# Kernel tuning notes

Measured on AMD Instinct MI355X. Metric: run time of the kernel, lower is better.

The kernel has to match this reference:

```python
import jax, jax.numpy as jnp
import numpy as np
from jax import lax

G = 64      # ngroup
CPN = 4     # channels per group in hidden layers
H, W = 32, 64
K = 5       # conv kernel
BIN = 8     # bin_num
BIAS = 3.5  # (bin_num-1)/2
NMIX = 3    # GMM components (batch replicas)
SCALE = 65536.0


def _group_mask(cout, cin, strict):
    # wavefront causality: tap (dg, di, dj) allowed iff dg+di+dj < 0 (strict) or <= 0
    g = jnp.arange(G)
    dg = g[None, :] - g[:, None]                      # (Gout, Gin)
    off = jnp.arange(K) - K // 2
    dd = off[:, None] + off[None, :]                  # (K, K)
    tot = dg[:, :, None, None] + dd[None, None, :, :]
    m = (tot < 0) if strict else (tot <= 0)
    m = jnp.repeat(jnp.repeat(m, cout, axis=0), cin, axis=1)
    return m.astype(jnp.float32)                      # (G*cout, G*cin, K, K)


def _cconv(x, w, b, m, relu):
    y = lax.conv_general_dilated(x, w * m, (1, 1), 'SAME',
                                 dimension_numbers=('NCHW', 'OIHW', 'NCHW'))
    y = y + b[None, :, None, None]
    return jax.nn.relu(y) if relu else y


def setup_inputs() -> dict:
    key = jax.random.key(0)
    ks = jax.random.split(key, 8)
    data = jax.random.randint(ks[0], (1, G, H, W), 0, BIN).astype(jnp.float32)
    mask = jax.random.randint(ks[1], (1, G, H, W), 0, 2).astype(jnp.float32)
    s = 0.05
    w_in = jax.random.normal(ks[2], (G * CPN, G, K, K), jnp.float32) * s
    b_in = jnp.zeros((G * CPN,), jnp.float32)
    w_hid = jax.random.normal(ks[3], (10, G * CPN, G * CPN, K, K), jnp.float32) * s
    b_hid = jnp.zeros((10, G * CPN), jnp.float32)
    w_out = jax.random.normal(ks[4], (G * NMIX, G * CPN, K, K), jnp.float32) * s
    b_out = jnp.zeros((G * NMIX,), jnp.float32)
    return dict(data=data, mask=mask, w_in=w_in, b_in=b_in,
                w_hid=w_hid, b_hid=b_hid, w_out=w_out, b_out=b_out)


def reference(data, mask, w_in, b_in, w_hid, b_hid, w_out, b_out):
    m_in = _group_mask(CPN, 1, True)      # first layer: strict (excludes current group)
    m_hid = _group_mask(CPN, CPN, False)
    m_out = _group_mask(NMIX, CPN, False)
    tdata = (data - BIAS) * mask
    x = jnp.concatenate([tdata, tdata, tdata], axis=0)   # (3, G, H, W)
    x = _cconv(x, w_in, b_in, m_in, True)
    for i in range(5):                                   # 5 residual blocks
        h = _cconv(x, w_hid[2 * i], b_hid[2 * i], m_hid, True)
        h = _cconv(h, w_hid[2 * i + 1], b_hid[2 * i + 1], m_hid, True)
        x = x + h
    y = _cconv(x, w_out, b_out, m_out, False)            # (3, G*3, H, W)
    y = y.reshape(NMIX, G, NMIX, H, W)                   # batch replica m -> mixture m
    logits = y[:, :, 0]
    mu = y[:, :, 1]
    sig = jax.nn.softplus(y[:, :, 2]) + 1e-6
    wts = jax.nn.softmax(logits, axis=0)                 # (3, G, H, W)
    edges = jnp.arange(BIN, dtype=jnp.float32) + 0.5 - BIAS
    z = (edges[:, None, None, None, None] - mu[None]) / (sig[None] * jnp.float32(np.sqrt(2.0)))
    cdf = 0.5 * (1.0 + lax.erf(z))                       # (BIN, 3, G, H, W)
    table = jnp.einsum('kmghw,mghw->ghwk', cdf, wts) * SCALE
    return table                                         # (G, H, W, BIN) quantizable CDF
```

## Files before the change

kernel.cpp:

```cpp
#include <hip/hip_runtime.h>
#include <math.h>

typedef _Float16 f16;
typedef _Float16 f16x8 __attribute__((ext_vector_type(8)));
typedef float f32x4 __attribute__((ext_vector_type(4)));

#define HH 32
#define WW 64
#define NPX 2048
#define SLOTS 68
#define CHS 78336
#define LOSCALE 2048.0f
#define INV_LOSCALE 4.8828125e-4f

typedef const __attribute__((address_space(1))) void gvoid;
typedef __attribute__((address_space(3))) void lvoid;
__device__ __forceinline__ void gload_lds16(const void* g, void* l) {
    __builtin_amdgcn_global_load_lds((gvoid*)g, (lvoid*)l, 16, 0, 0);
}

__global__ void zero_kernel(f16* p, int n8) {
    int i = blockIdx.x * 256 + threadIdx.x;
    if (i < n8) *(int4*)(p + i * 8) = make_int4(0, 0, 0, 0);
}

__global__ void prep_kernel(const float* __restrict__ data,
                            const float* __restrict__ mask,
                            f16* __restrict__ X0, int plane) {
    int idx = blockIdx.x * 256 + threadIdx.x;
    if (idx >= NPX * 64) return;
    int px = idx >> 6, ci = idx & 63;
    int hh = px >> 6, w = px & 63;
    float v = (data[ci * NPX + px] - 3.5f) * mask[ci * NPX + px];
    int dst = (ci >> 5) * CHS + ((hh + 2) * SLOTS + (w + 2)) * 32 + (ci & 31);
    X0[dst] = (f16)v;
    X0[plane + dst] = (f16)0.f;
}

__global__ void repack_kernel(const float* __restrict__ W, f16* __restrict__ WP,
                              int cin_log2, int coutp_log2,
                              int cpg_in_log2, int limb, int is_out) {
    int idx = blockIdx.x * 256 + threadIdx.x;
    int Cin = 1 << cin_log2;
    int plane = 25 << (cin_log2 + coutp_log2);
    int ci = idx & (Cin - 1);
    int rest = idx >> cin_log2;
    int co_p = rest & ((1 << coutp_log2) - 1);
    int tap = rest >> coutp_log2;
    if (tap >= 25) return;
    int ky = tap / 5, kx = tap - 5 * ky;
    int co_orig, g_out;
    if (is_out) { g_out = co_p >> 1; co_orig = 3 * g_out + 1 + (co_p & 1); }
    else        { g_out = co_p >> 2; co_orig = co_p; }
    int g_in = ci >> cpg_in_log2;
    float v = 0.f;
    if (ky + kx <= limb + g_out - g_in)
        v = W[(co_orig * Cin + ci) * 25 + tap];
    f16 vh = (f16)v;
    int dst = (((tap << (coutp_log2 - 4)) + (co_p >> 4)) << (cin_log2 - 5 + 9))
            + ((ci >> 5) << 9) + ((co_p & 15) << 5) + (ci & 31);
    WP[dst] = vh;
    WP[plane + dst] = (f16)((v - (float)vh) * LOSCALE);
}

__global__ __launch_bounds__(320, 3) void conv_kernel(
    const f16* __restrict__ IN, int Cin, int inPlane,
    const f16* __restrict__ WP, int wPlane,
    const float* __restrict__ bias,
    const f16* __restrict__ RES, int resPlane,
    f16* __restrict__ OA, int oaPlane,
    float* __restrict__ OT,
    int nmt, int Coutp, int cpg_out, int cpg_in, int limb, int mode)
{
    __shared__ __align__(16) char SMEM[46080];
    f16* BL = (f16*)SMEM;
    float* RED = (float*)SMEM;

    const int t = threadIdx.x;
    const int kw = t >> 6;
    const int lane = t & 63, l15 = lane & 15, q = lane >> 4;

    int b = blockIdx.x;
    int half = nmt << 4;
    int slot = b >= half ? 1 : 0;
    int idx = b - (slot ? half : 0);
    int mt8 = idx >> 5;
    const int h = idx & 31;
    const int mt = slot ? (nmt - 1 - mt8) : mt8;
    const int co0 = mt * 16;
    const int g_max = (co0 + 15) / cpg_out;

    int cnt[5];
#pragma unroll
    for (int kx = 0; kx < 5; kx++) {
        int c = (g_max + limb - (kw + kx) + 1) * cpg_in;
        c = c < Cin ? c : Cin;
        cnt[kx] = c > 0 ? c : 0;
    }
    int ci_top = (g_max + limb + 1) * cpg_in;
    ci_top = ci_top < Cin ? ci_top : Cin;

    const f16* src[9];
#pragma unroll
    for (int r = 0; r < 9; r++) {
        int u = r * 320 + t;
        if (u >= 2720) u = 0;
        int pl = u >= 1360 ? 1 : 0;
        int rem = u - pl * 1360;
        src[r] = IN + (size_t)pl * inPlane + h * 2176 + rem * 8;
    }

    f32x4 acc_h[4], acc_m[4];
#pragma unroll
    for (int j = 0; j < 4; j++) {
        acc_h[j] = (f32x4){0.f, 0.f, 0.f, 0.f};
        acc_m[j] = (f32x4){0.f, 0.f, 0.f, 0.f};
    }

    const size_t kxs = (size_t)Coutp * Cin;
    const f16* wb0 = WP + (size_t)(kw * 5 * (Coutp >> 4) + mt) * ((size_t)Cin << 4)
                   + l15 * 32 + q * 8;

    int coff = 0;
    for (int ci0 = 0; ci0 < ci_top; ci0 += 32, coff += CHS) {
        __syncthreads();
#pragma unroll
        for (int r = 0; r < 9; r++) {
            int ub = r * 320 + kw * 64;
            if (ub < 2720)
                gload_lds16(src[r] + coff, BL + ub * 8);
        }
        __syncthreads();

        const f16* wb = wb0 + (ci0 >> 5) * 512;
        f16x8 cah, cal, nah, nal;
        if (ci0 < cnt[0]) {
            cah = *(const f16x8*)(wb);
            cal = *(const f16x8*)(wb + wPlane);
        }
#pragma unroll
        for (int kx = 0; kx < 5; kx++) {
            if (ci0 >= cnt[kx]) break;
            if (kx < 4 && ci0 < cnt[kx + 1]) {
                nah = *(const f16x8*)(wb + (kx + 1) * kxs);
                nal = *(const f16x8*)(wb + (kx + 1) * kxs + wPlane);
            }
            f16x8 bh[4], bl[4];
#pragma unroll
            for (int j = 0; j < 4; j++) {
                int slt = j * 16 + l15 + kx;
                bh[j] = *(const f16x8*)&BL[(0 * 5 + kw) * (SLOTS * 32) + slt * 32 + q * 8];
                bl[j] = *(const f16x8*)&BL[(1 * 5 + kw) * (SLOTS * 32) + slt * 32 + q * 8];
            }
#pragma unroll
            for (int j = 0; j < 4; j++) {
                acc_h[j] = __builtin_amdgcn_mfma_f32_16x16x32_f16(cah, bh[j], acc_h[j], 0, 0, 0);
                acc_m[j] = __builtin_amdgcn_mfma_f32_16x16x32_f16(cah, bl[j], acc_m[j], 0, 0, 0);
                acc_m[j] = __builtin_amdgcn_mfma_f32_16x16x32_f16(cal, bh[j], acc_m[j], 0, 0, 0);
            }
            cah = nah; cal = nal;
        }
    }

    __syncthreads();
#pragma unroll
    for (int j = 0; j < 4; j++) {
        f32x4 v;
#pragma unroll
        for (int r = 0; r < 4; r++)
            v[r] = acc_h[j][r] + acc_m[j][r] * INV_LOSCALE;
        *(f32x4*)&RED[(kw * 64 + j * 16 + l15) * 20 + q * 4] = v;
    }
    __syncthreads();

    if (mode == 0) {
        for (int c = t; c < 1024; c += 320) {
            int px = c >> 4, col = c & 15;
            float v = bias[co0 + col];
#pragma unroll
            for (int k5 = 0; k5 < 5; k5++) v += RED[(k5 * 64 + px) * 20 + col];
            v = fmaxf(v, 0.f);
            int cc = co0 + col;
            int o = (cc >> 5) * CHS + ((h + 2) * SLOTS + px + 2) * 32 + (cc & 31);
            if (RES) v += (float)RES[o] + (float)RES[resPlane + o] * INV_LOSCALE;
            f16 vh = (f16)v;
            OA[o] = vh;
            OA[oaPlane + o] = (f16)((v - (float)vh) * LOSCALE);
        }
    } else {
        for (int c = t; c < 1024; c += 320) {
            int px = c >> 4, col = c & 15;
            float v = bias[3 * ((co0 + col) >> 1) + 1 + (col & 1)];
#pragma unroll
            for (int k5 = 0; k5 < 5; k5++) v += RED[(k5 * 64 + px) * 20 + col];
            RED[px * 20 + col] = v;
        }
        __syncthreads();
        for (int c = t; c < 512; c += 320) {
            int px = c >> 3, gl = c & 7;
            float mu = RED[px * 20 + 2 * gl];
            float s  = RED[px * 20 + 2 * gl + 1];
            float sp = fmaxf(s, 0.f) + log1pf(expf(-fabsf(s)));
            float sig = sp + 1e-6f;
            float inv = 1.f / (sig * 1.41421356237f);
            int g = (co0 >> 1) + gl;
            float* o = OT + ((size_t)g * NPX + h * WW + px) * 8;
#pragma unroll
            for (int k = 0; k < 8; k++) {
                float z = ((float)k - 3.0f - mu) * inv;
                o[k] = 32768.f * (1.f + erff(z));
            }
        }
    }
}

extern "C" void kernel_launch(void* const* d_in, const int* in_sizes, int n_in,
                              void* d_out, int out_size, void* d_ws, size_t ws_size,
                              hipStream_t stream) {
    const float* data  = (const float*)d_in[0];
    const float* mask  = (const float*)d_in[1];
    const float* w_in  = (const float*)d_in[2];
    const float* b_in  = (const float*)d_in[3];
    const float* w_hid = (const float*)d_in[4];
    const float* b_hid = (const float*)d_in[5];
    const float* w_out = (const float*)d_in[6];
    const float* b_out = (const float*)d_in[7];
    float* out = (float*)d_out;

    f16* WP = (f16*)d_ws;
    f16* P  = WP + 3276800;
    f16* Q  = P + 1253376;
    f16* X0 = Q + 1253376;

    zero_kernel<<<1377, 256, 0, stream>>>(P, 352512);
    prep_kernel<<<512, 256, 0, stream>>>(data, mask, X0, 156672);

    repack_kernel<<<1600, 256, 0, stream>>>(w_in, WP, 6, 8, 0, 3, 0);
    conv_kernel<<<512, 320, 0, stream>>>(X0, 64, 156672, WP, 409600,
        b_in, nullptr, 0, P, 626688, nullptr, 16, 256, 4, 1, 3, 0);

    for (int i = 0; i < 5; i++) {
        repack_kernel<<<6400, 256, 0, stream>>>(w_hid + (size_t)(2 * i) * 1638400,
                                                WP, 8, 8, 2, 4, 0);
        conv_kernel<<<512, 320, 0, stream>>>(P, 256, 626688, WP, 1638400,
            b_hid + 2 * i * 256, nullptr, 0, Q, 626688, nullptr, 16, 256, 4, 4, 4, 0);
        repack_kernel<<<6400, 256, 0, stream>>>(w_hid + (size_t)(2 * i + 1) * 1638400,
                                                WP, 8, 8, 2, 4, 0);
        conv_kernel<<<512, 320, 0, stream>>>(Q, 256, 626688, WP, 1638400,
            b_hid + (2 * i + 1) * 256, P, 626688, P, 626688, nullptr, 16, 256, 4, 4, 4, 0);
    }

    repack_kernel<<<3200, 256, 0, stream>>>(w_out, WP, 8, 7, 2, 4, 1);
    conv_kernel<<<256, 320, 0, stream>>>(P, 256, 626688, WP, 819200,
        b_out, nullptr, 0, nullptr, 0, out, 8, 128, 2, 4, 4, 1);
}
```

Baseline: 459.7 us.

## Pair complementary output tiles per block and double-buffer input loads

```diff
diff --git a/kernel.cpp b/kernel.cpp
--- a/kernel.cpp
+++ b/kernel.cpp
@@ -63,16 +63,16 @@
     WP[plane + dst] = (f16)((v - (float)vh) * LOSCALE);
 }
 
-__global__ __launch_bounds__(320, 3) void conv_kernel(
+__global__ __launch_bounds__(320, 2) void conv_kernel(
     const f16* __restrict__ IN, int Cin, int inPlane,
     const f16* __restrict__ WP, int wPlane,
     const float* __restrict__ bias,
     const f16* __restrict__ RES, int resPlane,
     f16* __restrict__ OA, int oaPlane,
     float* __restrict__ OT,
-    int nmt, int Coutp, int cpg_out, int cpg_in, int limb, int mode)
+    int nmt, int Coutp, int cpg_out, int cpg_in, int limb, int mode, int paired)
 {
-    __shared__ __align__(16) char SMEM[46080];
+    __shared__ __align__(16) char SMEM[92160];
     f16* BL = (f16*)SMEM;
     float* RED = (float*)SMEM;
 
@@ -80,108 +80,162 @@
     const int kw = t >> 6;
     const int lane = t & 63, l15 = lane & 15, q = lane >> 4;
 
-    int b = blockIdx.x;
-    int half = nmt << 4;
-    int slot = b >= half ? 1 : 0;
-    int idx = b - (slot ? half : 0);
-    int mt8 = idx >> 5;
-    const int h = idx & 31;
-    const int mt = slot ? (nmt - 1 - mt8) : mt8;
-    const int co0 = mt * 16;
-    const int g_max = (co0 + 15) / cpg_out;
-
-    int cnt[5];
+    const int nhalf = paired ? (nmt >> 1) : nmt;
+    const int mtp = blockIdx.x % nhalf;
+    const int h = blockIdx.x / nhalf;
+    const int mt1 = paired ? (nmt - 1 - mtp) : mtp;
+    const int mt0 = paired ? mtp : -1;
+
+    const int g1 = (mt1 * 16 + 15) / cpg_out;
+    const int g0 = mt0 >= 0 ? (mt0 * 16 + 15) / cpg_out : 0;
+
+    int cnt1[5], cnt0[5];
 #pragma unroll
     for (int kx = 0; kx < 5; kx++) {
-        int c = (g_max + limb - (kw + kx) + 1) * cpg_in;
+        int c = (g1 + limb - kw - kx + 1) * cpg_in;
         c = c < Cin ? c : Cin;
-        cnt[kx] = c > 0 ? c : 0;
-    }
-    int ci_top = (g_max + limb + 1) * cpg_in;
+        cnt1[kx] = c > 0 ? c : 0;
+        if (mt0 >= 0) {
+            int d = (g0 + limb - kw - kx + 1) * cpg_in;
+            d = d < Cin ? d : Cin;
+            cnt0[kx] = d > 0 ? d : 0;
+        } else cnt0[kx] = 0;
+    }
+    int ci_top = (g1 + limb + 1) * cpg_in;
     ci_top = ci_top < Cin ? ci_top : Cin;
-
-    const f16* src[9];
+    const int NT = (ci_top + 31) >> 5;
+
+    int soff[9];
 #pragma unroll
     for (int r = 0; r < 9; r++) {
         int u = r * 320 + t;
         if (u >= 2720) u = 0;
         int pl = u >= 1360 ? 1 : 0;
         int rem = u - pl * 1360;
-        src[r] = IN + (size_t)pl * inPlane + h * 2176 + rem * 8;
-    }
-
-    f32x4 acc_h[4], acc_m[4];
+        soff[r] = pl * inPlane + h * 2176 + rem * 8;
+    }
+
+    f32x4 a1h[4], a1m[4], a0h[4], a0m[4];
 #pragma unroll
     for (int j = 0; j < 4; j++) {
-        acc_h[j] = (f32x4){0.f, 0.f, 0.f, 0.f};
-        acc_m[j] = (f32x4){0.f, 0.f, 0.f, 0.f};
+        a1h[j] = (f32x4){0.f, 0.f, 0.f, 0.f};
+        a1m[j] = (f32x4){0.f, 0.f, 0.f, 0.f};
+        a0h[j] = (f32x4){0.f, 0.f, 0.f, 0.f};
+        a0m[j] = (f32x4){0.f, 0.f, 0.f, 0.f};
     }
 
     const size_t kxs = (size_t)Coutp * Cin;
-    const f16* wb0 = WP + (size_t)(kw * 5 * (Coutp >> 4) + mt) * ((size_t)Cin << 4)
+    const size_t tileStride = (size_t)Cin << 4;
+    const f16* w1b = WP + (size_t)(kw * 5 * (Coutp >> 4) + mt1) * tileStride
                    + l15 * 32 + q * 8;
-
-    int coff = 0;
-    for (int ci0 = 0; ci0 < ci_top; ci0 += 32, coff += CHS) {
-        __syncthreads();
-#pragma unroll
-        for (int r = 0; r < 9; r++) {
-            int ub = r * 320 + kw * 64;
-            if (ub < 2720)
-                gload_lds16(src[r] + coff, BL + ub * 8);
-        }
-        __syncthreads();
-
-        const f16* wb = wb0 + (ci0 >> 5) * 512;
-        f16x8 cah, cal, nah, nal;
-        if (ci0 < cnt[0]) {
-            cah = *(const f16x8*)(wb);
-            cal = *(const f16x8*)(wb + wPlane);
-        }
+    const f16* w0b = WP + (size_t)(kw * 5 * (Coutp >> 4) + (mt0 >= 0 ? mt0 : 0)) * tileStride
+                   + l15 * 32 + q * 8;
+
+#pragma unroll
+    for (int r = 0; r < 9; r++) {
+        int ub = r * 320 + kw * 64;
+        if (ub < 2720) gload_lds16(IN + soff[r], BL + ub * 8);
+    }
+
+    for (int it = 0; it < NT; ++it) {
+        const int ci0 = it << 5;
+        f16* buf = BL + (it & 1) * 23040;
+        const f16* w1 = w1b + it * 512;
+        const f16* w0 = w0b + it * 512;
+
+        f16x8 A1h[5], A1l[5], A0h[5], A0l[5];
+#pragma unroll
+        for (int kx = 0; kx < 4; kx++) {
+            A1h[kx] = *(const f16x8*)(w1 + kx * kxs);
+            A1l[kx] = *(const f16x8*)(w1 + kx * kxs + wPlane);
+            A0h[kx] = *(const f16x8*)(w0 + kx * kxs);
+            A0l[kx] = *(const f16x8*)(w0 + kx * kxs + wPlane);
+        }
+        asm volatile("s_waitcnt vmcnt(16)" ::: "memory");
+        __builtin_amdgcn_s_barrier();
+        asm volatile("" ::: "memory");
+
+        const f16* bhp = buf + kw * 2176 + q * 8;
+        const f16* blp = buf + 10880 + kw * 2176 + q * 8;
+
 #pragma unroll
         for (int kx = 0; kx < 5; kx++) {
-            if (ci0 >= cnt[kx]) break;
-            if (kx < 4 && ci0 < cnt[kx + 1]) {
-                nah = *(const f16x8*)(wb + (kx + 1) * kxs);
-                nal = *(const f16x8*)(wb + (kx + 1) * kxs + wPlane);
+            if (kx == 1 && it + 1 < NT) {
+                f16* nb = BL + ((it & 1) ^ 1) * 23040;
+                const int coff = (it + 1) * CHS;
+#pragma unroll
+                for (int r = 0; r < 9; r++) {
+                    int ub = r * 320 + kw * 64;
+                    if (ub < 2720) gload_lds16(IN + soff[r] + coff, nb + ub * 8);
+                }
             }
-            f16x8 bh[4], bl[4];
-#pragma unroll
-            for (int j = 0; j < 4; j++) {
-                int slt = j * 16 + l15 + kx;
-                bh[j] = *(const f16x8*)&BL[(0 * 5 + kw) * (SLOTS * 32) + slt * 32 + q * 8];
-                bl[j] = *(const f16x8*)&BL[(1 * 5 + kw) * (SLOTS * 32) + slt * 32 + q * 8];
+            if (kx == 2) {
+                if (ci0 < cnt1[4]) {
+                    A1h[4] = *(const f16x8*)(w1 + 4 * kxs);
+                    A1l[4] = *(const f16x8*)(w1 + 4 * kxs + wPlane);
+                }
+                if (ci0 < cnt0[4]) {
+                    A0h[4] = *(const f16x8*)(w0 + 4 * kxs);
+                    A0l[4] = *(const f16x8*)(w0 + 4 * kxs + wPlane);
+                }
             }
-#pragma unroll
-            for (int j = 0; j < 4; j++) {
-                acc_h[j] = __builtin_amdgcn_mfma_f32_16x16x32_f16(cah, bh[j], acc_h[j], 0, 0, 0);
-                acc_m[j] = __builtin_amdgcn_mfma_f32_16x16x32_f16(cah, bl[j], acc_m[j], 0, 0, 0);
-                acc_m[j] = __builtin_amdgcn_mfma_f32_16x16x32_f16(cal, bh[j], acc_m[j], 0, 0, 0);
+            if (ci0 < cnt1[kx]) {
+                f16x8 bh[4], bl[4];
+#pragma unroll
+                for (int j = 0; j < 4; j++) {
+                    int slt = j * 16 + l15 + kx;
+                    bh[j] = *(const f16x8*)(bhp + slt * 32);
+                    bl[j] = *(const f16x8*)(blp + slt * 32);
+                }
+#pragma unroll
+                for (int j = 0; j < 4; j++) {
+                    a1h[j] = __builtin_amdgcn_mfma_f32_16x16x32_f16(A1h[kx], bh[j], a1h[j], 0, 0, 0);
+                    a1m[j] = __builtin_amdgcn_mfma_f32_16x16x32_f16(A1h[kx], bl[j], a1m[j], 0, 0, 0);
+                    a1m[j] = __builtin_amdgcn_mfma_f32_16x16x32_f16(A1l[kx], bh[j], a1m[j], 0, 0, 0);
+                }
+                if (ci0 < cnt0[kx]) {
+#pragma unroll
+                    for (int j = 0; j < 4; j++) {
+                        a0h[j] = __builtin_amdgcn_mfma_f32_16x16x32_f16(A0h[kx], bh[j], a0h[j], 0, 0, 0);
+                        a0m[j] = __builtin_amdgcn_mfma_f32_16x16x32_f16(A0h[kx], bl[j], a0m[j], 0, 0, 0);
+                        a0m[j] = __builtin_amdgcn_mfma_f32_16x16x32_f16(A0l[kx], bh[j], a0m[j], 0, 0, 0);
+                    }
+                }
             }
-            cah = nah; cal = nal;
-        }
-    }
-
-    __syncthreads();
+        }
+        __builtin_amdgcn_s_barrier();
+        asm volatile("" ::: "memory");
+    }
+
 #pragma unroll
     for (int j = 0; j < 4; j++) {
         f32x4 v;
 #pragma unroll
         for (int r = 0; r < 4; r++)
-            v[r] = acc_h[j][r] + acc_m[j][r] * INV_LOSCALE;
-        *(f32x4*)&RED[(kw * 64 + j * 16 + l15) * 20 + q * 4] = v;
+            v[r] = a1h[j][r] + a1m[j][r] * INV_LOSCALE;
+        *(f32x4*)&RED[(kw * 64 + j * 16 + l15) * 36 + q * 4] = v;
+        if (mt0 >= 0) {
+            f32x4 u;
+#pragma unroll
+            for (int r = 0; r < 4; r++)
+                u[r] = a0h[j][r] + a0m[j][r] * INV_LOSCALE;
+            *(f32x4*)&RED[(kw * 64 + j * 16 + l15) * 36 + 16 + q * 4] = u;
+        }
     }
     __syncthreads();
 
     if (mode == 0) {
-        for (int c = t; c < 1024; c += 320) {
-            int px = c >> 4, col = c & 15;
-            float v = bias[co0 + col];
-#pragma unroll
-            for (int k5 = 0; k5 < 5; k5++) v += RED[(k5 * 64 + px) * 20 + col];
+        const int tot = mt0 >= 0 ? 2048 : 1024;
+        for (int c = t; c < tot; c += 320) {
+            int px, col;
+            if (mt0 >= 0) { px = c >> 5; col = c & 31; }
+            else          { px = c >> 4; col = c & 15; }
+            int co = col < 16 ? mt1 * 16 + col : mt0 * 16 + (col - 16);
+            float v = bias[co];
+#pragma unroll
+            for (int k5 = 0; k5 < 5; k5++) v += RED[(k5 * 64 + px) * 36 + col];
             v = fmaxf(v, 0.f);
-            int cc = co0 + col;
-            int o = (cc >> 5) * CHS + ((h + 2) * SLOTS + px + 2) * 32 + (cc & 31);
+            int o = (co >> 5) * CHS + ((h + 2) * SLOTS + px + 2) * 32 + (co & 31);
             if (RES) v += (float)RES[o] + (float)RES[resPlane + o] * INV_LOSCALE;
             f16 vh = (f16)v;
             OA[o] = vh;
@@ -190,20 +244,20 @@
     } else {
         for (int c = t; c < 1024; c += 320) {
             int px = c >> 4, col = c & 15;
-            float v = bias[3 * ((co0 + col) >> 1) + 1 + (col & 1)];
-#pragma unroll
-            for (int k5 = 0; k5 < 5; k5++) v += RED[(k5 * 64 + px) * 20 + col];
-            RED[px * 20 + col] = v;
+            float v = bias[3 * ((mt1 * 16 + col) >> 1) + 1 + (col & 1)];
+#pragma unroll
+            for (int k5 = 0; k5 < 5; k5++) v += RED[(k5 * 64 + px) * 36 + col];
+            RED[px * 36 + col] = v;
         }
         __syncthreads();
         for (int c = t; c < 512; c += 320) {
             int px = c >> 3, gl = c & 7;
-            float mu = RED[px * 20 + 2 * gl];
-            float s  = RED[px * 20 + 2 * gl + 1];
+            float mu = RED[px * 36 + 2 * gl];
+            float s  = RED[px * 36 + 2 * gl + 1];
             float sp = fmaxf(s, 0.f) + log1pf(expf(-fabsf(s)));
             float sig = sp + 1e-6f;
             float inv = 1.f / (sig * 1.41421356237f);
-            int g = (co0 >> 1) + gl;
+            int g = (mt1 * 16 >> 1) + gl;
             float* o = OT + ((size_t)g * NPX + h * WW + px) * 8;
 #pragma unroll
             for (int k = 0; k < 8; k++) {
@@ -236,21 +290,21 @@
     prep_kernel<<<512, 256, 0, stream>>>(data, mask, X0, 156672);
 
     repack_kernel<<<1600, 256, 0, stream>>>(w_in, WP, 6, 8, 0, 3, 0);
-    conv_kernel<<<512, 320, 0, stream>>>(X0, 64, 156672, WP, 409600,
-        b_in, nullptr, 0, P, 626688, nullptr, 16, 256, 4, 1, 3, 0);
+    conv_kernel<<<256, 320, 0, stream>>>(X0, 64, 156672, WP, 409600,
+        b_in, nullptr, 0, P, 626688, nullptr, 16, 256, 4, 1, 3, 0, 1);
 
     for (int i = 0; i < 5; i++) {
         repack_kernel<<<6400, 256, 0, stream>>>(w_hid + (size_t)(2 * i) * 1638400,
                                                 WP, 8, 8, 2, 4, 0);
-        conv_kernel<<<512, 320, 0, stream>>>(P, 256, 626688, WP, 1638400,
-            b_hid + 2 * i * 256, nullptr, 0, Q, 626688, nullptr, 16, 256, 4, 4, 4, 0);
+        conv_kernel<<<256, 320, 0, stream>>>(P, 256, 626688, WP, 1638400,
+            b_hid + 2 * i * 256, nullptr, 0, Q, 626688, nullptr, 16, 256, 4, 4, 4, 0, 1);
         repack_kernel<<<6400, 256, 0, stream>>>(w_hid + (size_t)(2 * i + 1) * 1638400,
                                                 WP, 8, 8, 2, 4, 0);
-        conv_kernel<<<512, 320, 0, stream>>>(Q, 256, 626688, WP, 1638400,
-            b_hid + (2 * i + 1) * 256, P, 626688, P, 626688, nullptr, 16, 256, 4, 4, 4, 0);
+        conv_kernel<<<256, 320, 0, stream>>>(Q, 256, 626688, WP, 1638400,
+            b_hid + (2 * i + 1) * 256, P, 626688, P, 626688, nullptr, 16, 256, 4, 4, 4, 0, 1);
     }
 
     repack_kernel<<<3200, 256, 0, stream>>>(w_out, WP, 8, 7, 2, 4, 1);
     conv_kernel<<<256, 320, 0, stream>>>(P, 256, 626688, WP, 819200,
-        b_out, nullptr, 0, nullptr, 0, out, 8, 128, 2, 4, 4, 1);
-}
+        b_out, nullptr, 0, nullptr, 0, out, 8, 128, 2, 4, 4, 1, 0);
+}
```

New measurement: 523.2 us. +13.8%, slower.
